# Optimization experiments

Hardware: AMD Instinct MI355X
Metric: run time of the kernel (lower is better)

The kernel has to match this reference:

```python
import jax, jax.numpy as jnp
import numpy as np

BATCH = 16384
N_MODES = 4096  # grid length == retained Fourier modes


def setup_inputs() -> dict:
    key = jax.random.key(0)
    k1, k2, k3 = jax.random.split(key, 3)
    inputs = jax.random.normal(k1, (BATCH, N_MODES), dtype=jnp.float32)
    # he_normal-style init for fourier weights, normal for linear weights
    fourier_weights = jax.random.normal(k2, (N_MODES,), dtype=jnp.float32) * np.sqrt(2.0 / N_MODES).astype(np.float32)
    linear_weights = jax.random.normal(k3, (N_MODES,), dtype=jnp.float32)
    return {"inputs": inputs, "fourier_weights": fourier_weights, "linear_weights": linear_weights}


def reference(inputs, fourier_weights, linear_weights):
    n_modes = fourier_weights.shape[0]
    # FFT along last axis (tf.signal.fft semantics), truncate to n_modes
    xf = jnp.fft.fft(inputs.astype(jnp.complex64), axis=-1)[:, :n_modes]
    # complex elementwise multiply by real weights cast to complex
    xf = xf * fourier_weights.astype(jnp.complex64)
    # inverse FFT over the truncated spectrum, take real part
    x = jnp.real(jnp.fft.ifft(xf, axis=-1)).astype(jnp.float32)
    # spectral branch scaled by linear weights + linear skip branch
    x = x * linear_weights
    z = inputs * linear_weights
    return jax.nn.relu(x + z)
```

## Files before the change

kernel.cpp:

```cpp
#include <hip/hip_runtime.h>
#include <math.h>

#define FFT_N   4096
#define THREADS 256
#define PADN    4352


#define REV(r) ((((r) & 3) << 2) | ((r) >> 2))

__global__ void setup_g_kernel(const float* __restrict__ fw, float* __restrict__ gperm) {
    int p = blockIdx.x * blockDim.x + threadIdx.x;
    if (p >= FFT_N) return;
    int r = p & 15;
    int local = (p & ~15) | REV(r);
    unsigned k = ((local & 15u) << 8) | ((unsigned)local & 0xF0u) | ((unsigned)local >> 8);
    float wk  = fw[k];
    float wnk = fw[(FFT_N - k) & (FFT_N - 1)];
    gperm[p] = (0.5f * (wk + wnk) + 1.0f) * (1.0f / (float)FFT_N);
}

__device__ __forceinline__ void cmul(float& xr, float& xi, float c, float s) {
    float tv = xr; xr = tv * c - xi * s; xi = tv * s + xi * c;
}

__device__ __forceinline__ void bfly4_f(float& ar, float& ai, float& br, float& bi,
                                        float& cr, float& ci, float& dr, float& di) {
    float t0r = ar + cr, t0i = ai + ci;
    float t1r = ar - cr, t1i = ai - ci;
    float t2r = br + dr, t2i = bi + di;
    float t3r = br - dr, t3i = bi - di;
    ar = t0r + t2r; ai = t0i + t2i;
    br = t1r + t3i; bi = t1i - t3r;
    cr = t0r - t2r; ci = t0i - t2i;
    dr = t1r - t3i; di = t1i + t3r;
}
__device__ __forceinline__ void bfly4_i(float& ar, float& ai, float& br, float& bi,
                                        float& cr, float& ci, float& dr, float& di) {
    float t0r = ar + cr, t0i = ai + ci;
    float t1r = ar - cr, t1i = ai - ci;
    float t2r = br + dr, t2i = bi + di;
    float t3r = br - dr, t3i = bi - di;
    ar = t0r + t2r; ai = t0i + t2i;
    br = t1r - t3i; bi = t1i + t3r;
    cr = t0r - t2r; ci = t0i - t2i;
    dr = t1r + t3i; di = t1i - t3r;
}

__device__ __forceinline__ void dft16_f(float xr[16], float xi[16]) {
    const float C1 = 0.9238795325112867f;
    const float S1 = 0.3826834323650898f;
    const float H  = 0.7071067811865476f;
    #pragma unroll
    for (int m = 0; m < 4; ++m)
        bfly4_f(xr[m],xi[m], xr[m+4],xi[m+4], xr[m+8],xi[m+8], xr[m+12],xi[m+12]);
    cmul(xr[5],  xi[5],   C1, -S1);
    cmul(xr[9],  xi[9],    H,  -H);
    cmul(xr[13], xi[13],  S1, -C1);
    cmul(xr[6],  xi[6],    H,  -H);
    cmul(xr[10], xi[10], 0.f, -1.f);
    cmul(xr[14], xi[14],  -H,  -H);
    cmul(xr[7],  xi[7],   S1, -C1);
    cmul(xr[11], xi[11],  -H,  -H);
    cmul(xr[15], xi[15], -C1,  S1);
    #pragma unroll
    for (int g = 0; g < 4; ++g)
        bfly4_f(xr[4*g],xi[4*g], xr[4*g+1],xi[4*g+1], xr[4*g+2],xi[4*g+2], xr[4*g+3],xi[4*g+3]);
}

__device__ __forceinline__ void idft16(float xr[16], float xi[16]) {
    const float C1 = 0.9238795325112867f;
    const float S1 = 0.3826834323650898f;
    const float H  = 0.7071067811865476f;
    #pragma unroll
    for (int g = 0; g < 4; ++g)
        bfly4_i(xr[4*g],xi[4*g], xr[4*g+1],xi[4*g+1], xr[4*g+2],xi[4*g+2], xr[4*g+3],xi[4*g+3]);
    cmul(xr[5],  xi[5],   C1,  S1);
    cmul(xr[9],  xi[9],    H,   H);
    cmul(xr[13], xi[13],  S1,  C1);
    cmul(xr[6],  xi[6],    H,   H);
    cmul(xr[10], xi[10], 0.f, 1.f);
    cmul(xr[14], xi[14],  -H,   H);
    cmul(xr[7],  xi[7],   S1,  C1);
    cmul(xr[11], xi[11],  -H,   H);
    cmul(xr[15], xi[15], -C1, -S1);
    #pragma unroll
    for (int m = 0; m < 4; ++m)
        bfly4_i(xr[m],xi[m], xr[m+4],xi[m+4], xr[m+8],xi[m+8], xr[m+12],xi[m+12]);
}

__device__ __forceinline__ void twiddle_rev(float xr[16], float xi[16], float ang) {
    float s1, c1; __sincosf(ang, &s1, &c1);
    float c2 = c1*c1 - s1*s1, s2 = 2.f*c1*s1;
    float c3 = c2*c1 - s2*s1, s3 = c2*s1 + s2*c1;
    float c4 = c2*c2 - s2*s2, s4 = 2.f*c2*s2;
    cmul(xr[4],  xi[4],  c1, s1);
    cmul(xr[8],  xi[8],  c2, s2);
    cmul(xr[12], xi[12], c3, s3);
    float bc = c4, bs = s4;
    #pragma unroll
    for (int q = 1; q < 4; ++q) {
        cmul(xr[q], xi[q], bc, bs);
        { float ec = bc*c1 - bs*s1, es = bc*s1 + bs*c1; cmul(xr[4+q],  xi[4+q],  ec, es); }
        { float ec = bc*c2 - bs*s2, es = bc*s2 + bs*c2; cmul(xr[8+q],  xi[8+q],  ec, es); }
        { float ec = bc*c3 - bs*s3, es = bc*s3 + bs*c3; cmul(xr[12+q], xi[12+q], ec, es); }
        if (q < 3) { float nb = bc*c4 - bs*s4; bs = bc*s4 + bs*c4; bc = nb; }
    }
}

__global__ __launch_bounds__(THREADS, 4) void fourier_fft_kernel(
    const float* __restrict__ in, const float* __restrict__ gperm,
    const float* __restrict__ lw, float* __restrict__ out)
{
    __shared__ __align__(16) float re[PADN];
    __shared__ __align__(16) float im[PADN];
    const int t = threadIdx.x;
    const long long pair = blockIdx.x;
    const float* r0 = in + pair * (2LL * FFT_N);
    const float* r1 = r0 + FFT_N;

    const float CFA = -6.28318530717958647692f / 4096.0f;
    const float CFB = -6.28318530717958647692f / 256.0f;

    const int baseA = t + 4 * (t >> 6);
    const int baseB = 272 * (t >> 4) + (t & 15);
    const int baseC = 16 * t + 4 * (t >> 2);
    const int jb = t & 15;

    float xr[16], xi[16];

    #pragma unroll
    for (int n = 0; n < 16; ++n) {
        xr[n] = r0[t + 256*n];
        xi[n] = r1[t + 256*n];
    }

    dft16_f(xr, xi);
    twiddle_rev(xr, xi, CFA * (float)t);
    #pragma unroll
    for (int k = 0; k < 16; ++k) {
        re[baseA + 272*k] = xr[REV(k)];
        im[baseA + 272*k] = xi[REV(k)];
    }
    __syncthreads();

    #pragma unroll
    for (int n = 0; n < 16; ++n) {
        int s = baseB + 16*n + 4*(n>>2);
        xr[n] = re[s]; xi[n] = im[s];
    }
    dft16_f(xr, xi);
    twiddle_rev(xr, xi, CFB * (float)jb);
    #pragma unroll
    for (int k = 0; k < 16; ++k) {
        int s = baseB + 16*k + 4*(k>>2);
        re[s] = xr[REV(k)]; im[s] = xi[REV(k)];
    }

    #pragma unroll
    for (int q = 0; q < 4; ++q) {
        float4 vr = *(const float4*)&re[baseC + 4*q];
        float4 vi = *(const float4*)&im[baseC + 4*q];
        xr[4*q+0] = vr.x; xr[4*q+1] = vr.y; xr[4*q+2] = vr.z; xr[4*q+3] = vr.w;
        xi[4*q+0] = vi.x; xi[4*q+1] = vi.y; xi[4*q+2] = vi.z; xi[4*q+3] = vi.w;
    }
    dft16_f(xr, xi);
    {
        const float4* gp = (const float4*)(gperm + 16*t);
        #pragma unroll
        for (int q = 0; q < 4; ++q) {
            float4 g = gp[q];
            xr[4*q+0] *= g.x; xi[4*q+0] *= g.x;
            xr[4*q+1] *= g.y; xi[4*q+1] *= g.y;
            xr[4*q+2] *= g.z; xi[4*q+2] *= g.z;
            xr[4*q+3] *= g.w; xi[4*q+3] *= g.w;
        }
    }
    idft16(xr, xi);
    #pragma unroll
    for (int q = 0; q < 4; ++q) {
        *(float4*)&re[baseC + 4*q] = make_float4(xr[4*q+0], xr[4*q+1], xr[4*q+2], xr[4*q+3]);
        *(float4*)&im[baseC + 4*q] = make_float4(xi[4*q+0], xi[4*q+1], xi[4*q+2], xi[4*q+3]);
    }

    #pragma unroll
    for (int k = 0; k < 16; ++k) {
        int s = baseB + 16*k + 4*(k>>2);
        xr[REV(k)] = re[s]; xi[REV(k)] = im[s];
    }
    twiddle_rev(xr, xi, -CFB * (float)jb);
    idft16(xr, xi);
    #pragma unroll
    for (int n = 0; n < 16; ++n) {
        int s = baseB + 16*n + 4*(n>>2);
        re[s] = xr[n]; im[s] = xi[n];
    }
    __syncthreads();

    #pragma unroll
    for (int k = 0; k < 16; ++k) {
        xr[REV(k)] = re[baseA + 272*k];
        xi[REV(k)] = im[baseA + 272*k];
    }
    twiddle_rev(xr, xi, -CFA * (float)t);
    idft16(xr, xi);

    float* o0 = out + pair * (2LL * FFT_N);
    #pragma unroll
    for (int n = 0; n < 16; ++n) {
        int i = t + 256*n;
        float l = lw[i];
        o0[i]         = fmaxf(xr[n]*l, 0.0f);
        o0[FFT_N + i] = fmaxf(xi[n]*l, 0.0f);
    }
}

extern "C" void kernel_launch(void* const* d_in, const int* in_sizes, int n_in,
                              void* d_out, int out_size, void* d_ws, size_t ws_size,
                              hipStream_t stream) {
    const float* inputs = (const float*)d_in[0];
    const float* fw     = (const float*)d_in[1];
    const float* lw     = (const float*)d_in[2];
    float* out   = (float*)d_out;
    float* gperm = (float*)d_ws;

    hipLaunchKernelGGL(setup_g_kernel, dim3(FFT_N / THREADS), dim3(THREADS), 0, stream,
                       fw, gperm);

    const int pairs = in_sizes[0] / (2 * FFT_N);
    hipLaunchKernelGGL(fourier_fft_kernel, dim3(pairs), dim3(THREADS), 0, stream,
                       inputs, gperm, lw, out);
}
```

Baseline: 116.2 us.

## Make FFT kernel persistent and prefetch next row pair into LDS asynchronously

Replaces the one-block-per-pair launch with a fixed grid of 512 persistent blocks that loop over pairs. Each block stages its input pair in a separate 32KB LDS buffer with direct global-to-LDS loads, and issues the next pair's load after the first exchange barrier so it overlaps the remaining FFT stages. This aims to hide global load latency behind compute. The cost is higher LDS use per block, which lowers occupancy, plus a fixed pair count that no longer follows the input size.

```diff
diff --git a/kernel.cpp b/kernel.cpp
--- a/kernel.cpp
+++ b/kernel.cpp
@@ -4,9 +4,16 @@
 #define FFT_N   4096
 #define THREADS 256
 #define PADN    4352
+#define GRID    512
+#define NPAIRS  8192
+#define ITERS   (NPAIRS / GRID)
+#define LDS_BYTES ((8192 + 2 * PADN) * 4)
 
 
 #define REV(r) ((((r) & 3) << 2) | ((r) >> 2))
+
+typedef const __attribute__((address_space(1))) unsigned int* gas_t;
+typedef __attribute__((address_space(3))) unsigned int* las_t;
 
 __global__ void setup_g_kernel(const float* __restrict__ fw, float* __restrict__ gperm) {
     int p = blockIdx.x * blockDim.x + threadIdx.x;
@@ -107,16 +114,17 @@
     }
 }
 
-__global__ __launch_bounds__(THREADS, 4) void fourier_fft_kernel(
+__global__ __launch_bounds__(THREADS) void fourier_fft_kernel(
     const float* __restrict__ in, const float* __restrict__ gperm,
     const float* __restrict__ lw, float* __restrict__ out)
 {
-    __shared__ __align__(16) float re[PADN];
-    __shared__ __align__(16) float im[PADN];
+    extern __shared__ __align__(16) float lds[];
+    float* S  = lds;
+    float* re = lds + 8192;
+    float* im = lds + 8192 + PADN;
+
     const int t = threadIdx.x;
-    const long long pair = blockIdx.x;
-    const float* r0 = in + pair * (2LL * FFT_N);
-    const float* r1 = r0 + FFT_N;
+    const int wv = t >> 6, ln = t & 63;
 
     const float CFA = -6.28318530717958647692f / 4096.0f;
     const float CFB = -6.28318530717958647692f / 256.0f;
@@ -125,92 +133,123 @@
     const int baseB = 272 * (t >> 4) + (t & 15);
     const int baseC = 16 * t + 4 * (t >> 2);
     const int jb = t & 15;
+    const float angA =  CFA * (float)t;
+    const float angB =  CFB * (float)jb;
 
     float xr[16], xi[16];
-
-    #pragma unroll
-    for (int n = 0; n < 16; ++n) {
-        xr[n] = r0[t + 256*n];
-        xi[n] = r1[t + 256*n];
-    }
-
-    dft16_f(xr, xi);
-    twiddle_rev(xr, xi, CFA * (float)t);
-    #pragma unroll
-    for (int k = 0; k < 16; ++k) {
-        re[baseA + 272*k] = xr[REV(k)];
-        im[baseA + 272*k] = xi[REV(k)];
+    long long pair = blockIdx.x;
+
+    {
+        const float* g0 = in + pair * (2LL * FFT_N);
+        #pragma unroll
+        for (int q = 0; q < 8; ++q) {
+            const int chunk = wv * 8 + q;
+            __builtin_amdgcn_global_load_lds(
+                (gas_t)(g0 + chunk * 256 + ln * 4),
+                (las_t)(S + chunk * 256), 16, 0, 0);
+        }
     }
     __syncthreads();
 
-    #pragma unroll
-    for (int n = 0; n < 16; ++n) {
-        int s = baseB + 16*n + 4*(n>>2);
-        xr[n] = re[s]; xi[n] = im[s];
-    }
-    dft16_f(xr, xi);
-    twiddle_rev(xr, xi, CFB * (float)jb);
-    #pragma unroll
-    for (int k = 0; k < 16; ++k) {
-        int s = baseB + 16*k + 4*(k>>2);
-        re[s] = xr[REV(k)]; im[s] = xi[REV(k)];
-    }
-
-    #pragma unroll
-    for (int q = 0; q < 4; ++q) {
-        float4 vr = *(const float4*)&re[baseC + 4*q];
-        float4 vi = *(const float4*)&im[baseC + 4*q];
-        xr[4*q+0] = vr.x; xr[4*q+1] = vr.y; xr[4*q+2] = vr.z; xr[4*q+3] = vr.w;
-        xi[4*q+0] = vi.x; xi[4*q+1] = vi.y; xi[4*q+2] = vi.z; xi[4*q+3] = vi.w;
-    }
-    dft16_f(xr, xi);
-    {
-        const float4* gp = (const float4*)(gperm + 16*t);
+    for (int it = 0; it < ITERS; ++it) {
+        #pragma unroll
+        for (int n = 0; n < 16; ++n) {
+            xr[n] = S[t + 256*n];
+            xi[n] = S[4096 + t + 256*n];
+        }
+        dft16_f(xr, xi);
+        twiddle_rev(xr, xi, angA);
+        #pragma unroll
+        for (int k = 0; k < 16; ++k) {
+            re[baseA + 272*k] = xr[REV(k)];
+            im[baseA + 272*k] = xi[REV(k)];
+        }
+        __syncthreads();
+
+        if (it + 1 < ITERS) {
+            const float* gn = in + (pair + GRID) * (2LL * FFT_N);
+            #pragma unroll
+            for (int q = 0; q < 8; ++q) {
+                const int chunk = wv * 8 + q;
+                __builtin_amdgcn_global_load_lds(
+                    (gas_t)(gn + chunk * 256 + ln * 4),
+                    (las_t)(S + chunk * 256), 16, 0, 0);
+            }
+        }
+
+        #pragma unroll
+        for (int n = 0; n < 16; ++n) {
+            int s = baseB + 16*n + 4*(n>>2);
+            xr[n] = re[s]; xi[n] = im[s];
+        }
+        dft16_f(xr, xi);
+        twiddle_rev(xr, xi, angB);
+        #pragma unroll
+        for (int k = 0; k < 16; ++k) {
+            int s = baseB + 16*k + 4*(k>>2);
+            re[s] = xr[REV(k)]; im[s] = xi[REV(k)];
+        }
+
         #pragma unroll
         for (int q = 0; q < 4; ++q) {
-            float4 g = gp[q];
-            xr[4*q+0] *= g.x; xi[4*q+0] *= g.x;
-            xr[4*q+1] *= g.y; xi[4*q+1] *= g.y;
-            xr[4*q+2] *= g.z; xi[4*q+2] *= g.z;
-            xr[4*q+3] *= g.w; xi[4*q+3] *= g.w;
-        }
-    }
-    idft16(xr, xi);
-    #pragma unroll
-    for (int q = 0; q < 4; ++q) {
-        *(float4*)&re[baseC + 4*q] = make_float4(xr[4*q+0], xr[4*q+1], xr[4*q+2], xr[4*q+3]);
-        *(float4*)&im[baseC + 4*q] = make_float4(xi[4*q+0], xi[4*q+1], xi[4*q+2], xi[4*q+3]);
-    }
-
-    #pragma unroll
-    for (int k = 0; k < 16; ++k) {
-        int s = baseB + 16*k + 4*(k>>2);
-        xr[REV(k)] = re[s]; xi[REV(k)] = im[s];
-    }
-    twiddle_rev(xr, xi, -CFB * (float)jb);
-    idft16(xr, xi);
-    #pragma unroll
-    for (int n = 0; n < 16; ++n) {
-        int s = baseB + 16*n + 4*(n>>2);
-        re[s] = xr[n]; im[s] = xi[n];
-    }
-    __syncthreads();
-
-    #pragma unroll
-    for (int k = 0; k < 16; ++k) {
-        xr[REV(k)] = re[baseA + 272*k];
-        xi[REV(k)] = im[baseA + 272*k];
-    }
-    twiddle_rev(xr, xi, -CFA * (float)t);
-    idft16(xr, xi);
-
-    float* o0 = out + pair * (2LL * FFT_N);
-    #pragma unroll
-    for (int n = 0; n < 16; ++n) {
-        int i = t + 256*n;
-        float l = lw[i];
-        o0[i]         = fmaxf(xr[n]*l, 0.0f);
-        o0[FFT_N + i] = fmaxf(xi[n]*l, 0.0f);
+            float4 vr = *(const float4*)&re[baseC + 4*q];
+            float4 vi = *(const float4*)&im[baseC + 4*q];
+            xr[4*q+0] = vr.x; xr[4*q+1] = vr.y; xr[4*q+2] = vr.z; xr[4*q+3] = vr.w;
+            xi[4*q+0] = vi.x; xi[4*q+1] = vi.y; xi[4*q+2] = vi.z; xi[4*q+3] = vi.w;
+        }
+        dft16_f(xr, xi);
+        {
+            const float4* gp = (const float4*)(gperm + 16*t);
+            #pragma unroll
+            for (int q = 0; q < 4; ++q) {
+                float4 g = gp[q];
+                xr[4*q+0] *= g.x; xi[4*q+0] *= g.x;
+                xr[4*q+1] *= g.y; xi[4*q+1] *= g.y;
+                xr[4*q+2] *= g.z; xi[4*q+2] *= g.z;
+                xr[4*q+3] *= g.w; xi[4*q+3] *= g.w;
+            }
+        }
+        idft16(xr, xi);
+        #pragma unroll
+        for (int q = 0; q < 4; ++q) {
+            *(float4*)&re[baseC + 4*q] = make_float4(xr[4*q+0], xr[4*q+1], xr[4*q+2], xr[4*q+3]);
+            *(float4*)&im[baseC + 4*q] = make_float4(xi[4*q+0], xi[4*q+1], xi[4*q+2], xi[4*q+3]);
+        }
+
+        #pragma unroll
+        for (int k = 0; k < 16; ++k) {
+            int s = baseB + 16*k + 4*(k>>2);
+            xr[REV(k)] = re[s]; xi[REV(k)] = im[s];
+        }
+        twiddle_rev(xr, xi, -angB);
+        idft16(xr, xi);
+        #pragma unroll
+        for (int n = 0; n < 16; ++n) {
+            int s = baseB + 16*n + 4*(n>>2);
+            re[s] = xr[n]; xi[n] = xi[n]; im[s] = xi[n];
+        }
+        __syncthreads();
+
+        #pragma unroll
+        for (int k = 0; k < 16; ++k) {
+            xr[REV(k)] = re[baseA + 272*k];
+            xi[REV(k)] = im[baseA + 272*k];
+        }
+        twiddle_rev(xr, xi, -angA);
+        idft16(xr, xi);
+        __syncthreads();
+
+        {
+            float* o0 = out + pair * (2LL * FFT_N);
+            #pragma unroll
+            for (int n = 0; n < 16; ++n) {
+                int i = t + 256*n;
+                float l = lw[i];
+                o0[i]         = fmaxf(xr[n]*l, 0.0f);
+                o0[FFT_N + i] = fmaxf(xi[n]*l, 0.0f);
+            }
+        }
+        pair += GRID;
     }
 }
 
@@ -223,10 +262,12 @@
     float* out   = (float*)d_out;
     float* gperm = (float*)d_ws;
 
+    (void)hipFuncSetAttribute((const void*)fourier_fft_kernel,
+                              hipFuncAttributeMaxDynamicSharedMemorySize, LDS_BYTES);
+
     hipLaunchKernelGGL(setup_g_kernel, dim3(FFT_N / THREADS), dim3(THREADS), 0, stream,
                        fw, gperm);
 
-    const int pairs = in_sizes[0] / (2 * FFT_N);
-    hipLaunchKernelGGL(fourier_fft_kernel, dim3(pairs), dim3(THREADS), 0, stream,
+    hipLaunchKernelGGL(fourier_fft_kernel, dim3(GRID), dim3(THREADS), LDS_BYTES, stream,
                        inputs, gperm, lw, out);
 }
```

New measurement: 171.5 us. 1.48x slower.
